# Performance work log

Hardware: AMD Instinct MI355X
Metric: run time of the kernel (lower is better)

The kernel has to match this reference:

```python
import jax, jax.numpy as jnp
import numpy as np

B, N, H, T = 128, 512, 128, 32


def setup_inputs() -> dict:
    key = jax.random.key(0)
    ks = jax.random.split(key, 6)
    s = 0.05  # small init scale keeps softmax logits sane
    return {
        "encoder_outputs": jax.random.normal(ks[0], (B, N, H), jnp.float32),
        "W_ih": jax.random.normal(ks[1], (4 * H, H), jnp.float32) * s,
        "W_hh": jax.random.normal(ks[2], (4 * H, H), jnp.float32) * s,
        "b_ih": jnp.zeros((4 * H,), jnp.float32),
        "b_hh": jnp.zeros((4 * H,), jnp.float32),
        "W1": jax.random.normal(ks[3], (H, H), jnp.float32) * s,
        "W2": jax.random.normal(ks[4], (H, H), jnp.float32) * s,
        "v": jax.random.normal(ks[5], (H,), jnp.float32) * s,
        "decode_steps": T,
    }


def reference(encoder_outputs, W_ih, W_hh, b_ih, b_hh, W1, W2, v, decode_steps):
    b, n, h = encoder_outputs.shape
    dtype = encoder_outputs.dtype
    # W1(encoder_outputs) is loop-invariant: hoist it (same math as the torch loop)
    enc_trans = jnp.einsum("bnh,kh->bnk", encoder_outputs, W1)  # [B,n,H]

    dec0 = encoder_outputs.mean(axis=1)  # [B,H]
    hx0 = jnp.zeros((b, h), dtype)
    cx0 = jnp.zeros((b, h), dtype)
    mask0 = jnp.zeros((b, n), bool)
    key0 = jax.random.key(42)
    rows = jnp.arange(b)

    def step(carry, _):
        dec_input, hx, cx, mask, key = carry
        # torch.nn.LSTMCell: gates ordered i, f, g, o
        gates = dec_input @ W_ih.T + b_ih + hx @ W_hh.T + b_hh  # [B,4H]
        i, f, g, o = jnp.split(gates, 4, axis=-1)
        i = jax.nn.sigmoid(i)
        f = jax.nn.sigmoid(f)
        g = jnp.tanh(g)
        o = jax.nn.sigmoid(o)
        cx_new = f * cx + i * g
        hx_new = o * jnp.tanh(cx_new)
        # additive attention scores
        dec_trans = hx_new @ W2.T  # [B,H]
        scores = jnp.einsum("bnh,h->bn", jnp.tanh(enc_trans + dec_trans[:, None, :]), v)
        scores = jnp.where(mask, -jnp.inf, scores)  # masked_fill(-inf)
        # sample next node (torch.multinomial on softmax == categorical on logits)
        key, sub = jax.random.split(key)
        idx = jax.random.categorical(sub, scores, axis=-1)  # [B]
        probs = jax.nn.softmax(scores, axis=-1)
        sel_log_prob = jnp.log(jnp.take_along_axis(probs, idx[:, None], axis=1)[:, 0] + 1e-9)
        mask_new = mask.at[rows, idx].set(True)
        dec_next = jnp.take_along_axis(encoder_outputs, idx[:, None, None], axis=1)[:, 0]  # [B,H]
        return (dec_next, hx_new, cx_new, mask_new, key), (idx, sel_log_prob)

    _, (tours, log_probs) = jax.lax.scan(
        step, (dec0, hx0, cx0, mask0, key0), xs=None, length=decode_steps
    )
    return tours.T, log_probs.T  # [B,T], [B,T]
```

## Files before the change

### kernel.cpp

```cpp
#include <hip/hip_runtime.h>
#include <cstdint>
#include <cstddef>


constexpr int B = 128, N = 512, H = 128, T = 32;
constexpr int G4 = 4 * H;
constexpr float TINYF = 1.17549435e-38f;

__host__ __device__ inline uint32_t rotl32(uint32_t v, int d) {
  return (v << d) | (v >> (32 - d));
}

__host__ __device__ inline void tf2x32(uint32_t k0, uint32_t k1,
                                       uint32_t x0, uint32_t x1,
                                       uint32_t& o0, uint32_t& o1) {
  uint32_t ks2 = k0 ^ k1 ^ 0x1BD11BDAu;
  x0 += k0; x1 += k1;
#define TF_R(r) x0 += x1; x1 = rotl32(x1, (r)); x1 ^= x0;
  TF_R(13) TF_R(15) TF_R(26) TF_R(6)
  x0 += k1; x1 += ks2 + 1u;
  TF_R(17) TF_R(29) TF_R(16) TF_R(24)
  x0 += ks2; x1 += k0 + 2u;
  TF_R(13) TF_R(15) TF_R(26) TF_R(6)
  x0 += k0; x1 += k1 + 3u;
  TF_R(17) TF_R(29) TF_R(16) TF_R(24)
  x0 += k1; x1 += ks2 + 4u;
  TF_R(13) TF_R(15) TF_R(26) TF_R(6)
  x0 += ks2; x1 += k0 + 5u;
#undef TF_R
  o0 = x0; o1 = x1;
}

struct KeyArgs { uint32_t k[2 * T]; };

static KeyArgs make_subkeys() {
  KeyArgs ka;
  uint32_t k0 = 0u, k1 = 42u;
  for (int t = 0; t < T; ++t) {
    uint32_t n0, n1, s0, s1;
    tf2x32(k0, k1, 0u, 0u, n0, n1);
    tf2x32(k0, k1, 0u, 1u, s0, s1);
    ka.k[2 * t] = s0; ka.k[2 * t + 1] = s1;
    k0 = n0; k1 = n1;
  }
  return ka;
}

__device__ inline uint32_t gumbel_bits(uint32_t sk0, uint32_t sk1, int i) {
  uint32_t o0, o1;
  tf2x32(sk0, sk1, 0u, (uint32_t)i, o0, o1);
  return o0 ^ o1;
}

__device__ inline float fast_tanh(float x) {
  float cx = fminf(9.0f, fmaxf(-9.0f, x));
  float t = __expf(2.0f * cx);
  return (t - 1.0f) * __builtin_amdgcn_rcpf(t + 1.0f);
}

__global__ void k_transpose(const float* __restrict__ Wih, const float* __restrict__ Whh,
                            const float* __restrict__ W2, const float* __restrict__ W1,
                            float* __restrict__ WihT, float* __restrict__ WhhT,
                            float* __restrict__ W2T, float* __restrict__ W1T) {
  int i = blockIdx.x * blockDim.x + threadIdx.x;
  if (i < H * G4) {
    int h = i >> 9, j = i & (G4 - 1);
    WihT[i] = Wih[j * H + h];
  } else if (i < 2 * H * G4) {
    int q = i - H * G4; int h = q >> 9, j = q & (G4 - 1);
    WhhT[q] = Whh[j * H + h];
  } else if (i < 2 * H * G4 + H * H) {
    int q = i - 2 * H * G4; int h = q >> 7, k = q & (H - 1);
    W2T[q] = W2[k * H + h];
  } else if (i < 2 * H * G4 + 2 * H * H) {
    int q = i - 2 * H * G4 - H * H; int h = q >> 7, k = q & (H - 1);
    W1T[q] = W1[k * H + h];
  }
}

__global__ __launch_bounds__(256) void k_enc_trans(const float* __restrict__ enc,
                                                   const float* __restrict__ W1T,
                                                   float* __restrict__ encT2) {
  __shared__ __align__(16) float es[16 * 128];
  int blk = blockIdx.x;
  int b = blk >> 5;
  int n0 = (blk & 31) << 4;
  const float* src = enc + ((size_t)b * N + n0) * H;
  for (int i = threadIdx.x; i < 16 * 128; i += 256) es[i] = src[i];
  __syncthreads();
  int k = threadIdx.x & 127, ng = threadIdx.x >> 7;
  float acc[8] = {0.f, 0.f, 0.f, 0.f, 0.f, 0.f, 0.f, 0.f};
  for (int h = 0; h < H; h += 4) {
    float w0 = W1T[(h + 0) * H + k];
    float w1 = W1T[(h + 1) * H + k];
    float w2 = W1T[(h + 2) * H + k];
    float w3 = W1T[(h + 3) * H + k];
#pragma unroll
    for (int j = 0; j < 8; ++j) {
      const float4 e = *(const float4*)&es[(ng * 8 + j) * 128 + h];
      acc[j] += w0 * e.x + w1 * e.y + w2 * e.z + w3 * e.w;
    }
  }
  float* dst = encT2 + (size_t)b * H * N + (size_t)k * N + n0 + ng * 8;
  ((float4*)dst)[0] = make_float4(acc[0], acc[1], acc[2], acc[3]);
  ((float4*)dst)[1] = make_float4(acc[4], acc[5], acc[6], acc[7]);
}

#define REP16(M) M(0) M(1) M(2) M(3) M(4) M(5) M(6) M(7) \
                 M(8) M(9) M(10) M(11) M(12) M(13) M(14) M(15)

__global__ __launch_bounds__(512)
__attribute__((amdgpu_waves_per_eu(2, 2))) void k_decode(
    const float* __restrict__ enc, const float* __restrict__ encT2,
    const float* __restrict__ WihT, const float* __restrict__ WhhT,
    const float* __restrict__ W2T,
    const float* __restrict__ bih, const float* __restrict__ bhh,
    const float* __restrict__ v,
    KeyArgs keys, float* __restrict__ out) {
  __shared__ __align__(16) float xs[H];
  __shared__ __align__(16) float hs[H];
  __shared__ __align__(16) float cs[H];
  __shared__ __align__(16) float dt[H];
  __shared__ __align__(16) float vv[H];
  __shared__ __align__(16) float bsum[G4];
  __shared__ float pg[G4];
  __shared__ float pdt[4][H];
  __shared__ float sc[N];
  __shared__ float wr_z[8], wr_m[8], wr_s[8];
  __shared__ int wr_i[8];

  extern __shared__ __align__(16) float e_lds[];

  const int tid = threadIdx.x;
  const int b = blockIdx.x;
  const int lane = tid & 63;
  const int wave = tid >> 6;

  const float* ep = encT2 + (size_t)b * (H * N) + tid;
#define ERLD(i) float4 er##i = make_float4(ep[(size_t)(4*i+0) * N], \
                                           ep[(size_t)(4*i+1) * N], \
                                           ep[(size_t)(4*i+2) * N], \
                                           ep[(size_t)(4*i+3) * N]);
  REP16(ERLD)
#undef ERLD

  {
    const float4* src4 = (const float4*)(encT2 + (size_t)b * (H * N) + (size_t)64 * N);
    float4* dst4 = (float4*)e_lds;
#pragma unroll
    for (int i = 0; i < 16; ++i) dst4[tid + i * 512] = src4[tid + i * 512];
  }

  {
    int h = tid & 127, part = tid >> 7;
    float s = 0.f;
    const float* p = enc + ((size_t)b * N + part * 128) * H + h;
#pragma unroll 8
    for (int n = 0; n < 128; ++n) s += p[(size_t)n * H];
    pdt[part][h] = s;
    bsum[tid] = bih[tid] + bhh[tid];
  }
  if (tid < 128) { hs[tid] = 0.f; cs[tid] = 0.f; vv[tid] = v[tid]; }
  __syncthreads();
  if (tid < 128)
    xs[tid] = (pdt[0][tid] + pdt[1][tid] + pdt[2][tid] + pdt[3][tid]) * (1.0f / N);
  bool masked = false;
  int sidx_r = 0;
  float smax_r = 0.f;
  __syncthreads();

  for (int t = 0; t < T; ++t) {
    {
      if (tid == 0 && t > 0) {
        float sum = wr_s[0] + wr_s[1] + wr_s[2] + wr_s[3]
                  + wr_s[4] + wr_s[5] + wr_s[6] + wr_s[7];
        float p = expf(sc[sidx_r] - smax_r) / sum;
        out[(size_t)b * T + (t - 1)] = (float)sidx_r;
        out[(size_t)B * T + (size_t)b * T + (t - 1)] = logf(p + 1e-9f);
      }
      const float* wi = WihT + tid;
      const float* wh = WhhT + tid;
      float a0x = 0.f, a0h = 0.f, a1x = 0.f, a1h = 0.f;
#pragma unroll 8
      for (int h = 0; h < 64; h += 4) {
        const float4 xv = *(const float4*)&xs[h];
        a0x += wi[(size_t)(h + 0) * G4] * xv.x;
        a0x += wi[(size_t)(h + 1) * G4] * xv.y;
        a0x += wi[(size_t)(h + 2) * G4] * xv.z;
        a0x += wi[(size_t)(h + 3) * G4] * xv.w;
        const float4 hv = *(const float4*)&hs[h];
        a0h += wh[(size_t)(h + 0) * G4] * hv.x;
        a0h += wh[(size_t)(h + 1) * G4] * hv.y;
        a0h += wh[(size_t)(h + 2) * G4] * hv.z;
        a0h += wh[(size_t)(h + 3) * G4] * hv.w;
      }
#pragma unroll 8
      for (int h = 64; h < 128; h += 4) {
        const float4 xv = *(const float4*)&xs[h];
        a1x += wi[(size_t)(h + 0) * G4] * xv.x;
        a1x += wi[(size_t)(h + 1) * G4] * xv.y;
        a1x += wi[(size_t)(h + 2) * G4] * xv.z;
        a1x += wi[(size_t)(h + 3) * G4] * xv.w;
        const float4 hv = *(const float4*)&hs[h];
        a1h += wh[(size_t)(h + 0) * G4] * hv.x;
        a1h += wh[(size_t)(h + 1) * G4] * hv.y;
        a1h += wh[(size_t)(h + 2) * G4] * hv.z;
        a1h += wh[(size_t)(h + 3) * G4] * hv.w;
      }
      pg[tid] = (a0x + a0h) + (a1x + a1h);
    }
    __syncthreads();
    if (tid < 128) {
      float gi = pg[tid] + bsum[tid];
      float gf = pg[H + tid] + bsum[H + tid];
      float gg = pg[2 * H + tid] + bsum[2 * H + tid];
      float go = pg[3 * H + tid] + bsum[3 * H + tid];
      gi = 1.0f / (1.0f + expf(-gi));
      gf = 1.0f / (1.0f + expf(-gf));
      gg = tanhf(gg);
      go = 1.0f / (1.0f + expf(-go));
      float c = gf * cs[tid] + gi * gg;
      cs[tid] = c;
      hs[tid] = go * tanhf(c);
    }
    __syncthreads();
    {
      int k = tid & 127, part = tid >> 7;
      const float* w2 = W2T + (size_t)(part * 32) * H + k;
      const int hbp = part * 32;
      float a = 0.f;
#pragma unroll 8
      for (int h = 0; h < 32; h += 4) {
        const float4 hv = *(const float4*)&hs[hbp + h];
        a += w2[(size_t)(h + 0) * H] * hv.x;
        a += w2[(size_t)(h + 1) * H] * hv.y;
        a += w2[(size_t)(h + 2) * H] * hv.z;
        a += w2[(size_t)(h + 3) * H] * hv.w;
      }
      pdt[part][k] = a;
    }
    __syncthreads();
    if (tid < 128) dt[tid] = pdt[0][tid] + pdt[1][tid] + pdt[2][tid] + pdt[3][tid];
    __syncthreads();
    float s;
    {
      float a0 = 0.f, a1 = 0.f;
#define P4A(i) { const float4 dv = *(const float4*)&dt[4 * i];              \
                 const float4 vw = *(const float4*)&vv[4 * i];              \
                 a0 += vw.x * fast_tanh(er##i.x + dv.x);                    \
                 a1 += vw.y * fast_tanh(er##i.y + dv.y);                    \
                 a0 += vw.z * fast_tanh(er##i.z + dv.z);                    \
                 a1 += vw.w * fast_tanh(er##i.w + dv.w); }
      REP16(P4A)
#undef P4A
      float b0 = 0.f, b1 = 0.f;
#pragma unroll
      for (int k4 = 0; k4 < 64; k4 += 4) {
        const float e0 = e_lds[(k4 + 0) * N + tid];
        const float e1 = e_lds[(k4 + 1) * N + tid];
        const float e2 = e_lds[(k4 + 2) * N + tid];
        const float e3 = e_lds[(k4 + 3) * N + tid];
        const float4 dv = *(const float4*)&dt[64 + k4];
        const float4 vw = *(const float4*)&vv[64 + k4];
        b0 += vw.x * fast_tanh(e0 + dv.x);
        b1 += vw.y * fast_tanh(e1 + dv.y);
        b0 += vw.z * fast_tanh(e2 + dv.z);
        b1 += vw.w * fast_tanh(e3 + dv.w);
      }
      const float s_score = (a0 + a1) + (b0 + b1);
      s = masked ? -INFINITY : s_score;
      sc[tid] = s;
      uint32_t bits = gumbel_bits(keys.k[2 * t], keys.k[2 * t + 1], b * N + tid);
      float f = __uint_as_float((bits >> 9) | 0x3f800000u) - 1.0f;
      float u = fmaxf(TINYF, f + TINYF);
      float g = -logf(-logf(u));
      float z = s + g;
      int zi = tid;
      float m = s;
#pragma unroll
      for (int d = 32; d >= 1; d >>= 1) {
        float oz = __shfl_xor(z, d);
        int oi = __shfl_xor(zi, d);
        float om = __shfl_xor(m, d);
        if (oz > z || (oz == z && oi < zi)) { z = oz; zi = oi; }
        m = fmaxf(m, om);
      }
      if (lane == 0) { wr_z[wave] = z; wr_i[wave] = zi; wr_m[wave] = m; }
    }
    __syncthreads();
    {
      float bz = wr_z[0]; int bi = wr_i[0]; float bm = wr_m[0];
#pragma unroll
      for (int w = 1; w < 8; ++w) {
        if (wr_z[w] > bz || (wr_z[w] == bz && wr_i[w] < bi)) { bz = wr_z[w]; bi = wr_i[w]; }
        bm = fmaxf(bm, wr_m[w]);
      }
      sidx_r = bi; smax_r = bm;
      float xnew = 0.f;
      if (tid < 128) xnew = enc[((size_t)b * N + bi) * H + tid];
      float e = expf(s - bm);
#pragma unroll
      for (int d = 32; d >= 1; d >>= 1) e += __shfl_xor(e, d);
      if (lane == 0) wr_s[wave] = e;
      if (tid == bi) masked = true;
      if (tid < 128) xs[tid] = xnew;
    }
    __syncthreads();
  }
  if (tid == 0) {
    float sum = wr_s[0] + wr_s[1] + wr_s[2] + wr_s[3]
              + wr_s[4] + wr_s[5] + wr_s[6] + wr_s[7];
    float p = expf(sc[sidx_r] - smax_r) / sum;
    out[(size_t)b * T + (T - 1)] = (float)sidx_r;
    out[(size_t)B * T + (size_t)b * T + (T - 1)] = logf(p + 1e-9f);
  }
}

extern "C" void kernel_launch(void* const* d_in, const int* in_sizes, int n_in,
                              void* d_out, int out_size, void* d_ws, size_t ws_size,
                              hipStream_t stream) {
  (void)in_sizes; (void)n_in; (void)out_size; (void)ws_size;
  const float* enc = (const float*)d_in[0];
  const float* Wih = (const float*)d_in[1];
  const float* Whh = (const float*)d_in[2];
  const float* bih = (const float*)d_in[3];
  const float* bhh = (const float*)d_in[4];
  const float* W1  = (const float*)d_in[5];
  const float* W2  = (const float*)d_in[6];
  const float* v   = (const float*)d_in[7];
  float* out = (float*)d_out;
  float* ws = (float*)d_ws;

  float* WihT  = ws;
  float* WhhT  = ws + 65536;
  float* W2T   = ws + 131072;
  float* W1T   = ws + 147456;
  float* encT2 = ws + 163840;

  KeyArgs keys = make_subkeys();

  static bool lds_attr_set = false;
  if (!lds_attr_set) {
    (void)hipFuncSetAttribute(reinterpret_cast<const void*>(k_decode),
                              hipFuncAttributeMaxDynamicSharedMemorySize, 131072);
    lds_attr_set = true;
  }

  k_transpose<<<640, 256, 0, stream>>>(Wih, Whh, W2, W1, WihT, WhhT, W2T, W1T);
  k_enc_trans<<<B * N / 16, 256, 0, stream>>>(enc, W1T, encT2);
  k_decode<<<B, 512, 131072, stream>>>(enc, encT2, WihT, WhhT, W2T,
                                       bih, bhh, v, keys, out);
}
```

Baseline: 580.5 us.

## Register-block enc_trans GEMM with packed W1 layout and 64-row tiles

Rewrites the encoder projection kernel so each thread computes a 4x8 output block instead of 1x8, reading W1 as float4 from a new packed layout written by the transpose kernel. Each block now stages 64 encoder rows in LDS with vectorised loads, and the grid is cut from 4096 to 1024 blocks. This cuts global weight loads and LDS reads per FMA, at the cost of more registers and 32KB of LDS per block, which may lower occupancy. The decode kernel probably dominates total time, so the overall effect may be small.

```diff
diff --git a/kernel.cpp b/kernel.cpp
--- a/kernel.cpp
+++ b/kernel.cpp
@@ -61,7 +61,7 @@
 __global__ void k_transpose(const float* __restrict__ Wih, const float* __restrict__ Whh,
                             const float* __restrict__ W2, const float* __restrict__ W1,
                             float* __restrict__ WihT, float* __restrict__ WhhT,
-                            float* __restrict__ W2T, float* __restrict__ W1T) {
+                            float* __restrict__ W2T, float* __restrict__ W1P) {
   int i = blockIdx.x * blockDim.x + threadIdx.x;
   if (i < H * G4) {
     int h = i >> 9, j = i & (G4 - 1);
@@ -73,37 +73,61 @@
     int q = i - 2 * H * G4; int h = q >> 7, k = q & (H - 1);
     W2T[q] = W2[k * H + h];
   } else if (i < 2 * H * G4 + 2 * H * H) {
-    int q = i - 2 * H * G4 - H * H; int h = q >> 7, k = q & (H - 1);
-    W1T[q] = W1[k * H + h];
+    int q = i - 2 * H * G4 - H * H;
+    int c = q & 3, k = (q >> 2) & 127, h4 = q >> 9;
+    W1P[q] = W1[k * H + h4 * 4 + c];
   }
 }
 
 __global__ __launch_bounds__(256) void k_enc_trans(const float* __restrict__ enc,
-                                                   const float* __restrict__ W1T,
+                                                   const float* __restrict__ W1P,
                                                    float* __restrict__ encT2) {
-  __shared__ __align__(16) float es[16 * 128];
-  int blk = blockIdx.x;
-  int b = blk >> 5;
-  int n0 = (blk & 31) << 4;
-  const float* src = enc + ((size_t)b * N + n0) * H;
-  for (int i = threadIdx.x; i < 16 * 128; i += 256) es[i] = src[i];
+  __shared__ __align__(16) float es[64 * 128];
+  const int blk = blockIdx.x;
+  const int b = blk >> 3;
+  const int n0 = (blk & 7) << 6;
+  const int tid = threadIdx.x;
+
+  {
+    const float4* src4 = (const float4*)(enc + ((size_t)b * N + n0) * H);
+    float4* dst4 = (float4*)es;
+#pragma unroll
+    for (int i = 0; i < 8; ++i) dst4[tid + i * 256] = src4[tid + i * 256];
+  }
   __syncthreads();
-  int k = threadIdx.x & 127, ng = threadIdx.x >> 7;
-  float acc[8] = {0.f, 0.f, 0.f, 0.f, 0.f, 0.f, 0.f, 0.f};
-  for (int h = 0; h < H; h += 4) {
-    float w0 = W1T[(h + 0) * H + k];
-    float w1 = W1T[(h + 1) * H + k];
-    float w2 = W1T[(h + 2) * H + k];
-    float w3 = W1T[(h + 3) * H + k];
-#pragma unroll
-    for (int j = 0; j < 8; ++j) {
-      const float4 e = *(const float4*)&es[(ng * 8 + j) * 128 + h];
-      acc[j] += w0 * e.x + w1 * e.y + w2 * e.z + w3 * e.w;
-    }
-  }
-  float* dst = encT2 + (size_t)b * H * N + (size_t)k * N + n0 + ng * 8;
-  ((float4*)dst)[0] = make_float4(acc[0], acc[1], acc[2], acc[3]);
-  ((float4*)dst)[1] = make_float4(acc[4], acc[5], acc[6], acc[7]);
+
+  const int kq = tid & 31;
+  const int ng = tid >> 5;
+  const float4* w4 = (const float4*)W1P + kq * 4;
+  const float4* es4 = (const float4*)es + ng * 8 * 32;
+
+  float acc[4][8];
+#pragma unroll
+  for (int i = 0; i < 4; ++i)
+#pragma unroll
+    for (int j = 0; j < 8; ++j) acc[i][j] = 0.f;
+
+  for (int h4 = 0; h4 < 32; ++h4) {
+    float4 wp[4];
+#pragma unroll
+    for (int i = 0; i < 4; ++i) wp[i] = w4[h4 * 128 + i];
+    float4 e[8];
+#pragma unroll
+    for (int j = 0; j < 8; ++j) e[j] = es4[j * 32 + h4];
+#pragma unroll
+    for (int i = 0; i < 4; ++i)
+#pragma unroll
+      for (int j = 0; j < 8; ++j)
+        acc[i][j] += wp[i].x * e[j].x + wp[i].y * e[j].y +
+                     wp[i].z * e[j].z + wp[i].w * e[j].w;
+  }
+
+#pragma unroll
+  for (int i = 0; i < 4; ++i) {
+    float* dst = encT2 + (size_t)b * (H * N) + (size_t)(kq * 4 + i) * N + n0 + ng * 8;
+    ((float4*)dst)[0] = make_float4(acc[i][0], acc[i][1], acc[i][2], acc[i][3]);
+    ((float4*)dst)[1] = make_float4(acc[i][4], acc[i][5], acc[i][6], acc[i][7]);
+  }
 }
 
 #define REP16(M) M(0) M(1) M(2) M(3) M(4) M(5) M(6) M(7) \
@@ -334,7 +358,7 @@
   float* WihT  = ws;
   float* WhhT  = ws + 65536;
   float* W2T   = ws + 131072;
-  float* W1T   = ws + 147456;
+  float* W1P   = ws + 147456;
   float* encT2 = ws + 163840;
 
   KeyArgs keys = make_subkeys();
@@ -346,8 +370,8 @@
     lds_attr_set = true;
   }
 
-  k_transpose<<<640, 256, 0, stream>>>(Wih, Whh, W2, W1, WihT, WhhT, W2T, W1T);
-  k_enc_trans<<<B * N / 16, 256, 0, stream>>>(enc, W1T, encT2);
+  k_transpose<<<640, 256, 0, stream>>>(Wih, Whh, W2, W1, WihT, WhhT, W2T, W1P);
+  k_enc_trans<<<B * 8, 256, 0, stream>>>(enc, W1P, encT2);
   k_decode<<<B, 512, 131072, stream>>>(enc, encT2, WihT, WhhT, W2T,
                                        bih, bhh, v, keys, out);
 }
```

New measurement: 573.8 us (median of 2 runs). Within noise of the previous version (-1.2%).
